# Optimization experiments

Measured on AMD Instinct MI355X. Metric: run time of the kernel, lower is better.

The kernel has to match this reference:

```python
import jax, jax.numpy as jnp
import numpy as np

D_MODEL = 2048
N_HEADS = 16
N_KV_HEADS = 4
DH = D_MODEL // N_HEADS          # 128
GROUPS = N_HEADS // N_KV_HEADS   # 4
ROPE_BASE = 10000.0
B, T = 2, 2048


def _rope_tables(positions):
    # positions: [T] int -> cos,sin [T, DH//2]
    inv = 1.0 / (ROPE_BASE ** (jnp.arange(0, DH, 2, dtype=jnp.float32) / DH))
    ang = positions.astype(jnp.float32)[:, None] * inv[None, :]
    return jnp.cos(ang), jnp.sin(ang)


def _apply_rope(x, cos, sin):
    # x: [B,H,T,DH]; cos/sin: [1,1,T,DH//2]; interleaved even/odd rotation
    even, odd = x[..., ::2], x[..., 1::2]
    xe = even * cos - odd * sin
    xo = even * sin + odd * cos
    return jnp.stack([xe, xo], axis=-1).reshape(x.shape)


def setup_inputs() -> dict:
    key = jax.random.key(0)
    k1, k2, k3 = jax.random.split(key, 3)
    qkv_dim = D_MODEL + 2 * N_KV_HEADS * DH
    x = jax.random.normal(k1, (B, T, D_MODEL), dtype=jnp.float32)
    Wqkv = jax.random.normal(k2, (D_MODEL, qkv_dim), dtype=jnp.float32) / np.sqrt(D_MODEL).astype(np.float32)
    Wo = jax.random.normal(k3, (N_HEADS * DH, D_MODEL), dtype=jnp.float32) / np.sqrt(N_HEADS * DH).astype(np.float32)
    return {"x": x, "Wqkv": Wqkv, "Wo": Wo, "start_pos": 0}


def reference(x, Wqkv, Wo, start_pos):
    Bx, Tx, _ = x.shape
    qkv = x @ Wqkv  # [B,T,D + 2*HKV*DH]
    q, k, v = jnp.split(qkv, [N_HEADS * DH, N_HEADS * DH + N_KV_HEADS * DH], axis=-1)
    q = q.reshape(Bx, Tx, N_HEADS, DH).transpose(0, 2, 1, 3)      # [B,H,T,DH]
    k = k.reshape(Bx, Tx, N_KV_HEADS, DH).transpose(0, 2, 1, 3)   # [B,HKV,T,DH]
    v = v.reshape(Bx, Tx, N_KV_HEADS, DH).transpose(0, 2, 1, 3)

    pos = start_pos + jnp.arange(Tx)
    cos, sin = _rope_tables(pos)
    cos = cos[None, None]; sin = sin[None, None]
    q = _apply_rope(q, cos, sin)
    k = _apply_rope(k, cos, sin)

    # GQA: repeat_interleave kv heads
    k = jnp.repeat(k, GROUPS, axis=1)  # [B,H,T,DH]
    v = jnp.repeat(v, GROUPS, axis=1)

    scale = 1.0 / np.sqrt(DH).astype(np.float32)
    att = jnp.einsum('bhqd,bhkd->bhqk', q, k) * scale
    causal = jnp.triu(jnp.ones((Tx, Tx), dtype=bool), 1)
    att = jnp.where(causal[None, None], jnp.float32(-jnp.inf), att)
    att = jax.nn.softmax(att, axis=-1)
    y = jnp.einsum('bhqk,bhkd->bhqd', att, v)
    y = y.transpose(0, 2, 1, 3).reshape(Bx, Tx, N_HEADS * DH)
    return y @ Wo
```

## Files before the change

kernel.cpp:

```cpp
#include <hip/hip_runtime.h>
#include <math.h>

#define D_MODEL 2048
#define N_HEADS 16
#define N_KV    4
#define DH      128
#define QKV_DIM 3072
#define TT      2048
#define BB      2
#define ROWS    (BB*TT)

#define QP_OFF 0u
#define KP_OFF 8388608u
#define VT_OFF 10485760u

typedef unsigned short u16;
typedef short short8 __attribute__((ext_vector_type(8)));
typedef short short4v __attribute__((ext_vector_type(4)));
typedef float float4v __attribute__((ext_vector_type(4)));

__device__ inline u16 f2b(float f) {
    union { float f; unsigned u; } v; v.f = f;
    unsigned r = v.u + 0x7FFF + ((v.u >> 16) & 1);
    return (u16)(r >> 16);
}

__device__ inline void async16(const void* g, void* l) {
    __builtin_amdgcn_global_load_lds(
        (const __attribute__((address_space(1))) void*)g,
        (__attribute__((address_space(3))) void*)l, 16, 0, 0);
}

__device__ inline void transpose_tile(const float* __restrict__ src,
                                      u16* __restrict__ dst,
                                      int R, int C, int col0,
                                      int bx, int by, u16* tile) {
    int bc = bx * 32, br = by * 32;
    int tx = threadIdx.x & 31, ty = threadIdx.x >> 5;
    for (int i = ty; i < 32; i += 8)
        tile[i * 33 + tx] = f2b(src[(size_t)(br + i) * C + col0 + bc + tx]);
    __syncthreads();
    for (int i = ty; i < 32; i += 8)
        dst[(size_t)(bc + i) * R + br + tx] = tile[tx * 33 + i];
}

__global__ __launch_bounds__(256) void prep_kernel(
    const float* __restrict__ x, u16* __restrict__ xb,
    const float* __restrict__ Wqkv, u16* __restrict__ WA, u16* __restrict__ WB) {
    __shared__ __align__(16) u16 tile[32 * 33];
    int bid = blockIdx.x;
    if (bid < 8192) {
        size_t i = (size_t)bid * 256 + threadIdx.x;
        float4v a = *(const float4v*)(x + i * 4);
        short4v p;
        p[0] = (short)f2b(a[0]); p[1] = (short)f2b(a[1]);
        p[2] = (short)f2b(a[2]); p[3] = (short)f2b(a[3]);
        *(short4v*)(xb + i * 4) = p;
    } else if (bid < 12288) {
        int t = bid - 8192;
        transpose_tile(Wqkv, WA, D_MODEL, QKV_DIM, 0, t & 63, t >> 6, tile);
    } else {
        int t = bid - 12288;
        transpose_tile(Wqkv, WB, D_MODEL, QKV_DIM, 2048, t & 31, t >> 5, tile);
    }
}

template<bool F32OUT, bool ROPE>
__global__ __launch_bounds__(256) void gemm_bt_async(
    const u16* __restrict__ A, const u16* __restrict__ Bt1, const u16* __restrict__ Bt2,
    int nsplit, void* __restrict__ Cv, int M, int N, int K, const int* __restrict__ sp) {
    __shared__ __align__(16) u16 As[128 * 32];
    __shared__ __align__(16) u16 Bs[128 * 32];
    const int tid = threadIdx.x;
    const int wave = tid >> 6, lane = tid & 63;
    const int quad = lane >> 4, l16 = lane & 15;
    const int bm = blockIdx.y * 128, bn = blockIdx.x * 128;
    const int wm = (wave >> 1) * 64, wn = (wave & 1) * 64;
    const int srow = wave * 32 + (lane >> 2);
    const int scol = (lane & 3) * 8;
    const u16* Bt = (bn < nsplit) ? (Bt1 + (size_t)bn * K)
                                  : (Bt2 + (size_t)(bn - nsplit) * K);

    float4v acc[4][4] = {};

    for (int k0 = 0; k0 < K; k0 += 32) {
        async16(A + (size_t)(bm + srow) * K + k0 + scol, (char*)As + wave * 2048);
        async16(A + (size_t)(bm + srow + 16) * K + k0 + scol, (char*)As + wave * 2048 + 1024);
        async16(Bt + (size_t)srow * K + k0 + scol, (char*)Bs + wave * 2048);
        async16(Bt + (size_t)(srow + 16) * K + k0 + scol, (char*)Bs + wave * 2048 + 1024);
        __syncthreads();
        short8 af[4], bf[4];
#pragma unroll
        for (int i = 0; i < 4; i++)
            af[i] = *(const short8*)(As + (wm + i * 16 + l16) * 32 + quad * 8);
#pragma unroll
        for (int j = 0; j < 4; j++)
            bf[j] = *(const short8*)(Bs + (wn + j * 16 + l16) * 32 + quad * 8);
#pragma unroll
        for (int i = 0; i < 4; i++)
#pragma unroll
            for (int j = 0; j < 4; j++)
                acc[i][j] = __builtin_amdgcn_mfma_f32_16x16x32_bf16(af[i], bf[j], acc[i][j], 0, 0, 0);
        __syncthreads();
    }
    const int sp0 = ROPE ? *sp : 0;
#pragma unroll
    for (int j = 0; j < 4; j++) {
        int col = bn + wn + j * 16 + l16;
        bool do_rope = ROPE && (col < 2560);
        float inv = 0.f;
        if (do_rope) inv = __expf(-0.14391156816f * (float)((col & 127) >> 1));
#pragma unroll
        for (int i = 0; i < 4; i++) {
            int row0 = bm + wm + i * 16 + quad * 4;
#pragma unroll
            for (int r = 0; r < 4; r++) {
                float v = acc[i][j][r];
                if (do_rope) {
                    float partner = __shfl_xor(v, 1, 64);
                    float ang = (float)(sp0 + ((row0 + r) & (TT - 1))) * inv;
                    float c = __cosf(ang), s = __sinf(ang);
                    v = (col & 1) ? (partner * s + v * c)
                                  : (v * c - partner * s);
                }
                if (F32OUT) {
                    ((float*)Cv)[(size_t)(row0 + r) * N + col] = v;
                } else {
                    int rw = row0 + r;
                    int bb = rw >> 11, t = rw & 2047;
                    size_t addr;
                    if (col < 2048)
                        addr = QP_OFF + (size_t)(bb * 16 + (col >> 7)) * 262144
                             + (size_t)t * 128 + (col & 127);
                    else if (col < 2560)
                        addr = KP_OFF + (size_t)(bb * 4 + ((col - 2048) >> 7)) * 262144
                             + (size_t)t * 128 + (col & 127);
                    else
                        addr = VT_OFF + (size_t)(bb * 4 + ((col - 2560) >> 7)) * 262144
                             + (size_t)(col & 127) * 2048 + t;
                    ((u16*)Cv)[addr] = f2b(v);
                }
            }
        }
    }
}

__global__ __launch_bounds__(256, 2) void attn_wo_kernel(
    const u16* __restrict__ qkv, u16* __restrict__ y,
    const float* __restrict__ Wo, u16* __restrict__ WoT) {
    __shared__ __align__(16) u16 Ks[2][32 * 128];
    __shared__ __align__(16) u16 Vs[2][128 * 32];
    __shared__ __align__(16) u16 Ps[4][32 * 32];

    if (blockIdx.x >= 512) {
        int t = blockIdx.x - 512;
        transpose_tile(Wo, WoT, D_MODEL, D_MODEL, 0, t & 63, t >> 6, (u16*)Ks[0]);
        return;
    }

    const int tid = threadIdx.x;
    const int wave = tid >> 6, lane = tid & 63;
    const int quad = lane >> 4, l16 = lane & 15;
    const int bx = blockIdx.x;
    const int xg = bx & 7;
    const int b = xg >> 2, hk = xg & 3;
    const int jj = bx >> 3;
    const int h = hk * 4 + 2 * ((jj >> 2) & 1) + (jj & 1);
    const int u = ((jj >> 1) & 1) | (((jj >> 3) & 1) << 1) | (((jj >> 4) & 1) << 2);
    const int p = ((jj >> 5) ^ jj) & 1;
    const int qt = p ? (15 - u) : u;
    const int g = b * 4 + hk;
    const float scale = 0.08838834764831845f;

    const int wq0 = qt * 128 + wave * 32;
    const u16* qbase = qkv + QP_OFF + (size_t)(b * 16 + h) * 262144;
    short8 qf[2][4];
#pragma unroll
    for (int gi = 0; gi < 2; gi++) {
        const u16* qrow = qbase + (size_t)(wq0 + gi * 16 + l16) * 128;
#pragma unroll
        for (int d = 0; d < 4; d++)
            qf[gi][d] = *(const short8*)(qrow + d * 32 + quad * 8);
    }

    float4v Oacc[2][8] = {};
    float4v Ol[2] = {};
    const short8 ONES = {(short)0x3F80, (short)0x3F80, (short)0x3F80, (short)0x3F80,
                         (short)0x3F80, (short)0x3F80, (short)0x3F80, (short)0x3F80};

    const int ktmax = 4 * qt + 3;

    size_t kg[2];
#pragma unroll
    for (int si = 0; si < 2; si++) {
        int kr = wave * 8 + si * 4 + quad;
        kg[si] = (size_t)kr * 128 + (size_t)((l16 ^ (kr & 7)) * 8);
    }
    size_t vg[2];
#pragma unroll
    for (int si = 0; si < 2; si++) {
        int vr = wave * 32 + si * 16 + (lane >> 2);
        vg[si] = (size_t)vr * 2048 + (size_t)((((lane & 3) ^ ((lane >> 3) & 3)) * 8));
    }
    const u16* Kb = qkv + KP_OFF + (size_t)g * 262144;
    const u16* Vb = qkv + VT_OFF + (size_t)g * 262144;

#pragma unroll
    for (int si = 0; si < 2; si++)
        async16(Kb + kg[si], (char*)Ks[0] + wave * 2048 + si * 1024);
#pragma unroll
    for (int si = 0; si < 2; si++)
        async16(Vb + vg[si], (char*)Vs[0] + wave * 2048 + si * 1024);

    for (int kt = 0; kt <= ktmax; kt++) {
        const int cur = kt & 1;
        __syncthreads();
        if (kt < ktmax) {
#pragma unroll
            for (int si = 0; si < 2; si++)
                async16(Kb + (size_t)(kt + 1) * 4096 + kg[si],
                        (char*)Ks[cur ^ 1] + wave * 2048 + si * 1024);
#pragma unroll
            for (int si = 0; si < 2; si++)
                async16(Vb + (size_t)(kt + 1) * 32 + vg[si],
                        (char*)Vs[cur ^ 1] + wave * 2048 + si * 1024);
        }
        const u16* Kcur = Ks[cur];
        const u16* Vcur = Vs[cur];

        float4v S[2][2] = {};
#pragma unroll
        for (int d = 0; d < 4; d++) {
#pragma unroll
            for (int j = 0; j < 2; j++) {
                short8 bk = *(const short8*)(Kcur + (j * 16 + l16) * 128
                                             + (((d * 4 + quad) ^ (l16 & 7)) * 8));
#pragma unroll
                for (int gi = 0; gi < 2; gi++)
                    S[gi][j] = __builtin_amdgcn_mfma_f32_16x16x32_bf16(qf[gi][d], bk, S[gi][j], 0, 0, 0);
            }
        }
        const int kvb = kt * 32 + l16;
        const bool diag = (kt * 32 + 31 > wq0);
#pragma unroll
        for (int gi = 0; gi < 2; gi++) {
            const int qbq = wq0 + gi * 16 + quad * 4;
#pragma unroll
            for (int j = 0; j < 2; j++)
#pragma unroll
                for (int r = 0; r < 4; r++) {
                    bool masked = diag && (kvb + j * 16 > qbq + r);
                    float pv = masked ? 0.f : __expf(S[gi][j][r] * scale);
                    int rq = gi * 16 + quad * 4 + r;
                    int ch = (j * 2 + (l16 >> 3)) ^ ((rq >> 1) & 3);
                    Ps[wave][rq * 32 + ch * 8 + (l16 & 7)] = f2b(pv);
                }
        }
        __asm__ volatile("s_waitcnt lgkmcnt(0)" ::: "memory");
        short8 ap[2];
#pragma unroll
        for (int gi = 0; gi < 2; gi++) {
            int rq = gi * 16 + l16;
            ap[gi] = *(const short8*)(Ps[wave] + rq * 32
                                      + ((quad ^ ((l16 >> 1) & 3)) * 8));
        }
#pragma unroll
        for (int dt = 0; dt < 8; dt++) {
            short8 bv = *(const short8*)(Vcur + (dt * 16 + l16) * 32
                                         + ((quad ^ ((l16 >> 1) & 3)) * 8));
#pragma unroll
            for (int gi = 0; gi < 2; gi++)
                Oacc[gi][dt] = __builtin_amdgcn_mfma_f32_16x16x32_bf16(ap[gi], bv, Oacc[gi][dt], 0, 0, 0);
        }
#pragma unroll
        for (int gi = 0; gi < 2; gi++)
            Ol[gi] = __builtin_amdgcn_mfma_f32_16x16x32_bf16(ap[gi], ONES, Ol[gi], 0, 0, 0);
    }
#pragma unroll
    for (int gi = 0; gi < 2; gi++)
#pragma unroll
        for (int dt = 0; dt < 8; dt++)
#pragma unroll
            for (int r = 0; r < 4; r++) {
                float v = Oacc[gi][dt][r] / Ol[gi][r];
                y[(size_t)(b * TT + wq0 + gi * 16 + quad * 4 + r) * D_MODEL
                  + h * 128 + dt * 16 + l16] = f2b(v);
            }
}

extern "C" void kernel_launch(void* const* d_in, const int* in_sizes, int n_in,
                              void* d_out, int out_size, void* d_ws, size_t ws_size,
                              hipStream_t stream) {
    const float* x    = (const float*)d_in[0];
    const float* Wqkv = (const float*)d_in[1];
    const float* Wo   = (const float*)d_in[2];
    const int*   sp   = (const int*)d_in[3];

    char* ws = (char*)d_ws;
    char* dob = (char*)d_out;
    u16*   xb     = (u16*)ws;
    u16*   Y      = (u16*)ws;
    u16*   WqkvTA = (u16*)(ws + 16777216);
    u16*   WoT    = (u16*)(ws + 16777216);
    u16*   QKVp   = (u16*)d_out;
    u16*   WqkvTB = (u16*)(dob + 25165824);
    float* out    = (float*)d_out;

    prep_kernel<<<14336, 256, 0, stream>>>(x, xb, Wqkv, WqkvTA, WqkvTB);
    gemm_bt_async<false, true><<<dim3(QKV_DIM / 128, ROWS / 128), 256, 0, stream>>>(
        xb, WqkvTA, WqkvTB, 2048, QKVp, ROWS, QKV_DIM, D_MODEL, sp);
    attn_wo_kernel<<<4608, 256, 0, stream>>>(QKVp, Y, Wo, WoT);
    gemm_bt_async<true, false><<<dim3(D_MODEL / 128, ROWS / 128), 256, 0, stream>>>(
        Y, WoT, WoT, D_MODEL, out, ROWS, D_MODEL, D_MODEL, sp);
}
```

Measured before the change: 331.6 us.

## Replace QKV GEMM with 256x256 tile, 8-wave phased pipelined kernel

Adds a dedicated QKV projection kernel that uses 256x256 block tiles, 512 threads, and double-buffered LDS with XOR-swizzled async loads. Loads are interleaved with MFMA phases under barriers and priority hints. RoPE and the head-scatter epilogue are fused as before. The intent is better data reuse and latency hiding than the generic 128x128 GEMM. The risk is that the grid shrinks to 192 blocks, which underfills the CUs, and that the large LDS footprint limits occupancy.

```diff
diff --git a/kernel.cpp b/kernel.cpp
--- a/kernel.cpp
+++ b/kernel.cpp
@@ -62,6 +62,130 @@
     } else {
         int t = bid - 12288;
         transpose_tile(Wqkv, WB, D_MODEL, QKV_DIM, 2048, t & 31, t >> 5, tile);
+    }
+}
+
+__global__ __launch_bounds__(512, 2) void gemm1_8ph(
+    const u16* __restrict__ A, const u16* __restrict__ Bt1,
+    const u16* __restrict__ Bt2, u16* __restrict__ Cv,
+    const int* __restrict__ sp) {
+    const int K = 2048, NT = 32;
+    __shared__ __align__(16) u16 As[2][256 * 64];
+    __shared__ __align__(16) u16 Bs[2][256 * 64];
+    const int tid = threadIdx.x;
+    const int wave = tid >> 6, lane = tid & 63;
+    const int quad = lane >> 4, l16 = lane & 15;
+    const int gm = wave >> 2, gn = wave & 3;
+    const int bm = blockIdx.y * 256, bn = blockIdx.x * 256;
+    const u16* Ag = A + (size_t)bm * K;
+    const u16* Bt = (bn < 2048) ? (Bt1 + (size_t)bn * K)
+                                : (Bt2 + (size_t)(bn - 2048) * K);
+
+    const int srl = lane >> 3;
+    const int sch = (lane & 7) ^ srl;
+
+    auto stage = [&](const u16* src, int half, u16* ldsTile) {
+#pragma unroll
+        for (int i = 0; i < 2; i++) {
+            int r0 = half * 128 + (wave * 2 + i) * 8;
+            async16(src + (size_t)(r0 + srl) * K + sch * 8,
+                    (char*)ldsTile + (size_t)r0 * 128);
+        }
+    };
+    auto ldfrag = [&](const u16* tile, int row16, int kk) -> short8 {
+        return *(const short8*)(tile + (size_t)(row16 + l16) * 64
+                                + (((kk * 4 + quad) ^ (l16 & 7)) * 8));
+    };
+
+    float4v acc[8][4] = {};
+    short8 bf[4][2];
+
+    stage(Ag, 0, As[0]); stage(Ag, 1, As[0]);
+    stage(Bt, 0, Bs[0]); stage(Bt, 1, Bs[0]);
+    stage(Bt + 64, 0, Bs[1]); stage(Bt + 64, 1, Bs[1]);
+    asm volatile("s_waitcnt vmcnt(4)" ::: "memory");
+    __builtin_amdgcn_s_barrier();
+
+    for (int t = 0; t < NT; t++) {
+        const int cur = t & 1;
+        const u16* Atile = As[cur] + gm * 128 * 64;
+        const u16* Btile = Bs[cur] + gn * 64 * 64;
+#pragma unroll
+        for (int q = 0; q < 4; q++) {
+            short8 af[2][2];
+            if (q == 0) {
+#pragma unroll
+                for (int cf = 0; cf < 4; cf++)
+#pragma unroll
+                    for (int kk = 0; kk < 2; kk++)
+                        bf[cf][kk] = ldfrag(Btile, cf * 16, kk);
+            }
+#pragma unroll
+            for (int i = 0; i < 2; i++)
+#pragma unroll
+                for (int kk = 0; kk < 2; kk++)
+                    af[i][kk] = ldfrag(Atile, (q * 2 + i) * 16, kk);
+            if (q == 0)      { if (t + 1 < NT) stage(Ag + (size_t)(t + 1) * 64, 0, As[cur ^ 1]); }
+            else if (q == 1) { if (t + 1 < NT) stage(Ag + (size_t)(t + 1) * 64, 1, As[cur ^ 1]); }
+            else if (q == 2) { if (t + 2 < NT) stage(Bt + (size_t)(t + 2) * 64, 0, Bs[cur]); }
+            else             { if (t + 2 < NT) stage(Bt + (size_t)(t + 2) * 64, 1, Bs[cur]); }
+            __builtin_amdgcn_sched_barrier(0);
+            __builtin_amdgcn_s_barrier();
+            asm volatile("s_waitcnt lgkmcnt(0)" ::: "memory");
+            __builtin_amdgcn_sched_barrier(0);
+            __builtin_amdgcn_s_setprio(1);
+#pragma unroll
+            for (int i = 0; i < 2; i++)
+#pragma unroll
+                for (int cf = 0; cf < 4; cf++)
+#pragma unroll
+                    for (int kk = 0; kk < 2; kk++)
+                        acc[q * 2 + i][cf] = __builtin_amdgcn_mfma_f32_16x16x32_bf16(
+                            af[i][kk], bf[cf][kk], acc[q * 2 + i][cf], 0, 0, 0);
+            __builtin_amdgcn_s_setprio(0);
+            if (q == 3) {
+                if (t < NT - 2)       asm volatile("s_waitcnt vmcnt(4)" ::: "memory");
+                else if (t == NT - 2) asm volatile("s_waitcnt vmcnt(0)" ::: "memory");
+            }
+            __builtin_amdgcn_s_barrier();
+        }
+    }
+
+    const int sp0 = *sp;
+#pragma unroll
+    for (int cf = 0; cf < 4; cf++) {
+        int col = bn + gn * 64 + cf * 16 + l16;
+        bool do_rope = (col < 2560);
+        float inv = 0.f;
+        if (do_rope) inv = __expf(-0.14391156816f * (float)((col & 127) >> 1));
+#pragma unroll
+        for (int rf = 0; rf < 8; rf++) {
+            int row0 = bm + gm * 128 + rf * 16 + quad * 4;
+#pragma unroll
+            for (int r = 0; r < 4; r++) {
+                float v = acc[rf][cf][r];
+                if (do_rope) {
+                    float partner = __shfl_xor(v, 1, 64);
+                    float ang = (float)(sp0 + ((row0 + r) & (TT - 1))) * inv;
+                    float c = __cosf(ang), s = __sinf(ang);
+                    v = (col & 1) ? (partner * s + v * c)
+                                  : (v * c - partner * s);
+                }
+                int rw = row0 + r;
+                int bb = rw >> 11, tt = rw & 2047;
+                size_t addr;
+                if (col < 2048)
+                    addr = QP_OFF + (size_t)(bb * 16 + (col >> 7)) * 262144
+                         + (size_t)tt * 128 + (col & 127);
+                else if (col < 2560)
+                    addr = KP_OFF + (size_t)(bb * 4 + ((col - 2048) >> 7)) * 262144
+                         + (size_t)tt * 128 + (col & 127);
+                else
+                    addr = VT_OFF + (size_t)(bb * 4 + ((col - 2560) >> 7)) * 262144
+                         + (size_t)(col & 127) * 2048 + tt;
+                Cv[addr] = f2b(v);
+            }
+        }
     }
 }
 
@@ -307,8 +431,8 @@
     float* out    = (float*)d_out;
 
     prep_kernel<<<14336, 256, 0, stream>>>(x, xb, Wqkv, WqkvTA, WqkvTB);
-    gemm_bt_async<false, true><<<dim3(QKV_DIM / 128, ROWS / 128), 256, 0, stream>>>(
-        xb, WqkvTA, WqkvTB, 2048, QKVp, ROWS, QKV_DIM, D_MODEL, sp);
+    gemm1_8ph<<<dim3(QKV_DIM / 256, ROWS / 256), 512, 0, stream>>>(
+        xb, WqkvTA, WqkvTB, QKVp, sp);
     attn_wo_kernel<<<4608, 256, 0, stream>>>(QKVp, Y, Wo, WoT);
     gemm_bt_async<true, false><<<dim3(D_MODEL / 128, ROWS / 128), 256, 0, stream>>>(
         Y, WoT, WoT, D_MODEL, out, ROWS, D_MODEL, D_MODEL, sp);
```

After: 349.4 us. 1.05x slower.
